# Kernel optimization log

Hardware: AMD Instinct MI355X
Metric: run time of the kernel (lower is better)

The kernel has to match this reference:

```python
import jax, jax.numpy as jnp
import numpy as np

N_NODES = 50000
N_EDGES = 800000
ATOM_DIM = 128
BOND_DIM = 16
HID = 128
STEPS = 4


def setup_inputs() -> dict:
    key = jax.random.key(0)
    k1, k2, k3, k4, k5, k6 = jax.random.split(key, 6)
    atoms = jax.random.normal(k1, (N_NODES, ATOM_DIM), dtype=jnp.float32)
    bonds = jax.random.normal(k2, (N_NODES, BOND_DIM), dtype=jnp.float32)
    pairs = jax.random.randint(k3, (N_EDGES, 2), 0, N_NODES)
    # sort rows by target id (tf.math.segment_sum expects sorted segment ids)
    order = jnp.argsort(pairs[:, 0])
    pairs = pairs[order].astype(jnp.int64)
    # learned parameters (glorot-ish scaling)
    kernel = jax.random.normal(k4, (ATOM_DIM, BOND_DIM * BOND_DIM), dtype=jnp.float32) * (2.0 / (ATOM_DIM + BOND_DIM * BOND_DIM)) ** 0.5
    bias = jnp.zeros((BOND_DIM * BOND_DIM,), dtype=jnp.float32)
    weight_node = jax.random.normal(k5, (BOND_DIM, HID), dtype=jnp.float32) * (2.0 / (BOND_DIM + HID)) ** 0.5
    weight_node_inp = jax.random.normal(k6, (BOND_DIM, HID), dtype=jnp.float32) * (2.0 / (BOND_DIM + HID)) ** 0.5
    return {"atoms": atoms, "bonds": bonds, "pairs": pairs,
            "kernel": kernel, "bias": bias,
            "weight_node": weight_node, "weight_node_inp": weight_node_inp}


def reference(atoms, bonds, pairs, kernel, bias, weight_node, weight_node_inp):
    n, bd = bonds.shape
    # per-node transform -> [N, bd, bd] message matrices
    A = (atoms @ kernel + bias).reshape(n, bd, bd)
    src = pairs[:, 0]
    nbr = pairs[:, 1]
    # gather bonds of neighbors, apply source-node matrix per edge: [E, bd]
    trans = jnp.einsum('eij,ej->ei', A[src], bonds[nbr])
    # scatter-add back to nodes keyed on pairs[:,0]
    aggregate = jax.ops.segment_sum(trans, src, num_segments=n)  # [N, bd]
    # step loop: aggregate is never updated in the original, so each step
    # computes the identical result; compute once and replicate.
    nodes = aggregate @ weight_node            # [N, hid]
    edges = jax.nn.relu(bonds @ weight_node_inp)  # [N, hid]
    result = jax.nn.relu(nodes + edges)
    return jnp.stack([result] * STEPS)  # [steps, N, hid]
```

## Files before the change

### kernel.cpp

```cpp
#include <hip/hip_runtime.h>

typedef __attribute__((ext_vector_type(8))) short bf16x8;
typedef __attribute__((ext_vector_type(4))) float f32x4;

constexpr int N       = 50000;
constexpr int NE      = 800000;
constexpr int AD      = 128;
constexpr int BD      = 16;
constexpr int BD2     = 256;
constexpr int HIDDEN  = 128;
constexpr int EPG     = 32;
constexpr int NB      = 64;

__device__ inline short f2bf(float f) {
    union U { float f; unsigned u; } v; v.f = f;
    unsigned r = v.u + 0x7fffu + ((v.u >> 16) & 1u);
    return (short)(r >> 16);
}

__global__ __launch_bounds__(256) void prep_frags(
    const float* __restrict__ kmat,
    const float* __restrict__ Wn,
    const float* __restrict__ Wi,
    short* __restrict__ kbf,
    short* __restrict__ wbf)
{
    int t = blockIdx.x * 256 + threadIdx.x;
    if (t < 4096) {
        int u = t >> 6, l = t & 63;
        int nf = u >> 2, kk = u & 3;
        int col = nf * 16 + (l & 15);
        int k0  = kk * 32 + (l >> 4) * 8;
        bf16x8 o;
#pragma unroll
        for (int j = 0; j < 8; ++j) o[j] = f2bf(kmat[(size_t)(k0 + j) * BD2 + col]);
        *(bf16x8*)(kbf + (size_t)t * 8) = o;
    } else if (t < 4096 + 1024) {
        int t2 = t - 4096;
        int u = t2 >> 6, l = t2 & 63;
        int m = u >> 3, nf2 = u & 7;
        const float* W = m ? Wi : Wn;
        int col = nf2 * 16 + (l & 15);
        int k0  = (l >> 4) * 8;
        bf16x8 o;
#pragma unroll
        for (int j = 0; j < 8; ++j) {
            int k = k0 + j;
            o[j] = (k < 16) ? f2bf(W[(size_t)k * HIDDEN + col]) : (short)0;
        }
        *(bf16x8*)(wbf + (size_t)t2 * 8) = o;
    }
}

__global__ __launch_bounds__(256) void edge_scatter_sorted(
    const int2* __restrict__ pairs,
    const float* __restrict__ bonds,
    float* __restrict__ S)
{
    const int gid = (int)((blockIdx.x * (unsigned)blockDim.x + threadIdx.x) >> 4);
    const int c   = threadIdx.x & 15;
    long e0 = (long)gid * EPG;
    if (e0 >= NE) return;

    int   cur = -1;
    float acc = 0.f;
    for (long e = e0; e < e0 + EPG; e += 4) {
        int2 pb[4]; float vb[4];
#pragma unroll
        for (int i = 0; i < 4; ++i) pb[i] = pairs[e + i];
#pragma unroll
        for (int i = 0; i < 4; ++i) vb[i] = bonds[(size_t)pb[i].y * BD + c];
#pragma unroll
        for (int i = 0; i < 4; ++i) {
            if (pb[i].x != cur) {
                if (cur >= 0) atomicAdd(&S[(size_t)cur * BD + c], acc);
                acc = 0.f;
                cur = pb[i].x;
            }
            acc += vb[i];
        }
    }
    atomicAdd(&S[(size_t)cur * BD + c], acc);
}

__global__ __launch_bounds__(256, 3) void fused_node_mfma(
    const float* __restrict__ atoms,
    const float* __restrict__ bonds,
    const short* __restrict__ kbf,
    const short* __restrict__ wbf,
    const float* __restrict__ bias,
    const float* __restrict__ S,
    float* __restrict__ out)
{
    const int tid = threadIdx.x;
    const int w   = tid >> 6;
    const int l   = tid & 63;
    const int lq  = l >> 4;
    const int lj  = l & 15;
    const int wrow = blockIdx.x * NB + w * 16;

    int arow = wrow + lj; if (arow >= N) arow = N - 1;
    const float* ap = atoms + (size_t)arow * AD + lq * 8;
    bf16x8 afrag[4];
#pragma unroll
    for (int kk = 0; kk < 4; ++kk) {
        float4 a0 = *(const float4*)(ap + kk * 32);
        float4 a1 = *(const float4*)(ap + kk * 32 + 4);
        bf16x8 af;
        af[0] = f2bf(a0.x); af[1] = f2bf(a0.y); af[2] = f2bf(a0.z); af[3] = f2bf(a0.w);
        af[4] = f2bf(a1.x); af[5] = f2bf(a1.y); af[6] = f2bf(a1.z); af[7] = f2bf(a1.w);
        afrag[kk] = af;
    }

    f32x4 acc[16];
#pragma unroll
    for (int nf = 0; nf < 16; ++nf) acc[nf] = (f32x4){0.f, 0.f, 0.f, 0.f};

    const bf16x8* kb = (const bf16x8*)kbf;
#pragma unroll 1
    for (int kk = 0; kk < 4; ++kk) {
#pragma unroll
        for (int nf = 0; nf < 16; ++nf) {
            bf16x8 b = kb[(size_t)(nf * 4 + kk) * 64 + l];
            acc[nf] = __builtin_amdgcn_mfma_f32_16x16x32_bf16(b, afrag[kk], acc[nf], 0, 0, 0);
        }
    }

    int srow = wrow + lj; if (srow >= N) srow = N - 1;
    float4 sv = *(const float4*)(S + (size_t)srow * BD + lq * 4);

    float aggf[16];
#pragma unroll
    for (int nf = 0; nf < 16; ++nf) {
        float4 bv = *(const float4*)(bias + nf * 16 + lq * 4);
        float q = (acc[nf][0] + bv.x) * sv.x
                + (acc[nf][1] + bv.y) * sv.y
                + (acc[nf][2] + bv.z) * sv.z
                + (acc[nf][3] + bv.w) * sv.w;
        q += __shfl_xor(q, 16);
        q += __shfl_xor(q, 32);
        aggf[nf] = q;
    }

    bf16x8 agg_a = (bf16x8){0,0,0,0,0,0,0,0};
    bf16x8 bond_a = (bf16x8){0,0,0,0,0,0,0,0};
    if (lq < 2) {
#pragma unroll
        for (int j = 0; j < 8; ++j) agg_a[j] = f2bf(aggf[lq * 8 + j]);
        int brow = wrow + lj; if (brow >= N) brow = N - 1;
        float4 b0 = *(const float4*)(bonds + (size_t)brow * BD + lq * 8);
        float4 b1 = *(const float4*)(bonds + (size_t)brow * BD + lq * 8 + 4);
        bond_a[0] = f2bf(b0.x); bond_a[1] = f2bf(b0.y); bond_a[2] = f2bf(b0.z); bond_a[3] = f2bf(b0.w);
        bond_a[4] = f2bf(b1.x); bond_a[5] = f2bf(b1.y); bond_a[6] = f2bf(b1.z); bond_a[7] = f2bf(b1.w);
    }

    const bf16x8* wb = (const bf16x8*)wbf;
#pragma unroll
    for (int nf2 = 0; nf2 < 8; ++nf2) {
        bf16x8 wn_f = wb[(size_t)nf2 * 64 + l];
        bf16x8 wi_f = wb[(size_t)(8 + nf2) * 64 + l];
        f32x4 e = __builtin_amdgcn_mfma_f32_16x16x32_bf16(
            bond_a, wi_f, (f32x4){0.f, 0.f, 0.f, 0.f}, 0, 0, 0);
        e[0] = fmaxf(e[0], 0.f); e[1] = fmaxf(e[1], 0.f);
        e[2] = fmaxf(e[2], 0.f); e[3] = fmaxf(e[3], 0.f);
        f32x4 o = __builtin_amdgcn_mfma_f32_16x16x32_bf16(agg_a, wn_f, e, 0, 0, 0);
#pragma unroll
        for (int r = 0; r < 4; ++r) {
            int node = wrow + 4 * lq + r;
            if (node < N) {
                float v = fmaxf(o[r], 0.f);
                size_t base = (size_t)node * HIDDEN + nf2 * 16 + lj;
#pragma unroll
                for (int s = 0; s < 4; ++s)
                    out[base + (size_t)s * N * HIDDEN] = v;
            }
        }
    }
}

extern "C" void kernel_launch(void* const* d_in, const int* in_sizes, int n_in,
                              void* d_out, int out_size, void* d_ws, size_t ws_size,
                              hipStream_t stream)
{
    const float* atoms = (const float*)d_in[0];
    const float* bonds = (const float*)d_in[1];
    const int2*  pairs = (const int2*)d_in[2];
    const float* kmat  = (const float*)d_in[3];
    const float* bias  = (const float*)d_in[4];
    const float* Wn    = (const float*)d_in[5];
    const float* Wi    = (const float*)d_in[6];
    float* out = (float*)d_out;

    float* S   = (float*)d_ws;
    short* kbf = (short*)((char*)d_ws + (size_t)N * BD * 4);
    short* wbf = kbf + 4096 * 8;

    hipMemsetAsync(S, 0, (size_t)N * BD * sizeof(float), stream);
    prep_frags<<<20, 256, 0, stream>>>(kmat, Wn, Wi, kbf, wbf);

    const int groups  = NE / EPG;
    const int threads = groups * 16;
    edge_scatter_sorted<<<(threads + 255) / 256, 256, 0, stream>>>(pairs, bonds, S);

    fused_node_mfma<<<(N + NB - 1) / NB, 256, 0, stream>>>(
        atoms, bonds, kbf, wbf, bias, S, out);
}
```

Measured before the change: 71.91 us.

## Fuse edge segment-sum into node kernel via binary search and LDS accumulation

```diff
diff --git a/kernel.cpp b/kernel.cpp
--- a/kernel.cpp
+++ b/kernel.cpp
@@ -9,8 +9,9 @@
 constexpr int BD      = 16;
 constexpr int BD2     = 256;
 constexpr int HIDDEN  = 128;
-constexpr int EPG     = 32;
 constexpr int NB      = 64;
+constexpr int SSTR    = 20;
+constexpr int OSTR    = 132;
 
 __device__ inline short f2bf(float f) {
     union U { float f; unsigned u; } v; v.f = f;
@@ -52,63 +53,102 @@
     }
 }
 
-__global__ __launch_bounds__(256) void edge_scatter_sorted(
-    const int2* __restrict__ pairs,
-    const float* __restrict__ bonds,
-    float* __restrict__ S)
-{
-    const int gid = (int)((blockIdx.x * (unsigned)blockDim.x + threadIdx.x) >> 4);
-    const int c   = threadIdx.x & 15;
-    long e0 = (long)gid * EPG;
-    if (e0 >= NE) return;
-
-    int   cur = -1;
-    float acc = 0.f;
-    for (long e = e0; e < e0 + EPG; e += 4) {
-        int2 pb[4]; float vb[4];
-#pragma unroll
-        for (int i = 0; i < 4; ++i) pb[i] = pairs[e + i];
-#pragma unroll
-        for (int i = 0; i < 4; ++i) vb[i] = bonds[(size_t)pb[i].y * BD + c];
-#pragma unroll
-        for (int i = 0; i < 4; ++i) {
-            if (pb[i].x != cur) {
-                if (cur >= 0) atomicAdd(&S[(size_t)cur * BD + c], acc);
-                acc = 0.f;
-                cur = pb[i].x;
-            }
-            acc += vb[i];
-        }
-    }
-    atomicAdd(&S[(size_t)cur * BD + c], acc);
-}
-
-__global__ __launch_bounds__(256, 3) void fused_node_mfma(
+__global__ __launch_bounds__(256, 4) void fused_all(
     const float* __restrict__ atoms,
     const float* __restrict__ bonds,
+    const int*  __restrict__ pairs,
     const short* __restrict__ kbf,
     const short* __restrict__ wbf,
     const float* __restrict__ bias,
-    const float* __restrict__ S,
     float* __restrict__ out)
 {
+    __shared__ float lds[NB * OSTR];
+
     const int tid = threadIdx.x;
     const int w   = tid >> 6;
     const int l   = tid & 63;
     const int lq  = l >> 4;
     const int lj  = l & 15;
-    const int wrow = blockIdx.x * NB + w * 16;
+    const int nb  = blockIdx.x * NB;
+    const int wrow = nb + w * 16;
 
     int arow = wrow + lj; if (arow >= N) arow = N - 1;
     const float* ap = atoms + (size_t)arow * AD + lq * 8;
+    float4 a0[4], a1[4];
+#pragma unroll
+    for (int kk = 0; kk < 4; ++kk) {
+        a0[kk] = *(const float4*)(ap + kk * 32);
+        a1[kk] = *(const float4*)(ap + kk * 32 + 4);
+    }
+
+    int wlo = nb * 16 - 4096; if (wlo < 0) wlo = 0;
+    int whi = (nb + NB) * 16 + 4096; if (whi > NE) whi = NE;
+    if (wlo > 0  && pairs[2 * wlo] >= nb)      wlo = 0;
+    if (whi < NE && pairs[2 * whi] <  nb + NB) whi = NE;
+    int eLo;
+    {
+        int s = wlo, e = whi;
+        while (s < e) { int m = (s + e) >> 1; if (pairs[2 * m] < nb) s = m + 1; else e = m; }
+        eLo = s;
+    }
+    int eHi;
+    {
+        int s = eLo, e = whi;
+        while (s < e) { int m = (s + e) >> 1; if (pairs[2 * m] < nb + NB) s = m + 1; else e = m; }
+        eHi = s;
+    }
+
+    for (int i = tid; i < NB * SSTR; i += 256) lds[i] = 0.f;
+    __syncthreads();
+
+    {
+        const int g = tid >> 4;
+        const int c = tid & 15;
+        const int nE = eHi - eLo;
+        const int cg = (nE + 15) >> 4;
+        int gs = eLo + g * cg;
+        int ge = gs + cg; if (ge > eHi) ge = eHi;
+        int cur = -1; float acc = 0.f;
+        int e = gs;
+        for (; e + 4 <= ge; e += 4) {
+            int2 pb[4]; float vb[4];
+#pragma unroll
+            for (int i = 0; i < 4; ++i) pb[i] = *(const int2*)(pairs + 2 * (e + i));
+#pragma unroll
+            for (int i = 0; i < 4; ++i) vb[i] = bonds[(size_t)pb[i].y * BD + c];
+#pragma unroll
+            for (int i = 0; i < 4; ++i) {
+                if (pb[i].x != cur) {
+                    if (cur >= 0) atomicAdd(&lds[(cur - nb) * SSTR + c], acc);
+                    acc = 0.f; cur = pb[i].x;
+                }
+                acc += vb[i];
+            }
+        }
+        for (; e < ge; ++e) {
+            int2 p = *(const int2*)(pairs + 2 * e);
+            float v = bonds[(size_t)p.y * BD + c];
+            if (p.x != cur) {
+                if (cur >= 0) atomicAdd(&lds[(cur - nb) * SSTR + c], acc);
+                acc = 0.f; cur = p.x;
+            }
+            acc += v;
+        }
+        if (cur >= 0) atomicAdd(&lds[(cur - nb) * SSTR + c], acc);
+    }
+    __syncthreads();
+
+    float4 sv = *(const float4*)(&lds[(w * 16 + lj) * SSTR + lq * 4]);
+    __syncthreads();
+
     bf16x8 afrag[4];
 #pragma unroll
     for (int kk = 0; kk < 4; ++kk) {
-        float4 a0 = *(const float4*)(ap + kk * 32);
-        float4 a1 = *(const float4*)(ap + kk * 32 + 4);
         bf16x8 af;
-        af[0] = f2bf(a0.x); af[1] = f2bf(a0.y); af[2] = f2bf(a0.z); af[3] = f2bf(a0.w);
-        af[4] = f2bf(a1.x); af[5] = f2bf(a1.y); af[6] = f2bf(a1.z); af[7] = f2bf(a1.w);
+        af[0] = f2bf(a0[kk].x); af[1] = f2bf(a0[kk].y);
+        af[2] = f2bf(a0[kk].z); af[3] = f2bf(a0[kk].w);
+        af[4] = f2bf(a1[kk].x); af[5] = f2bf(a1[kk].y);
+        af[6] = f2bf(a1[kk].z); af[7] = f2bf(a1[kk].w);
         afrag[kk] = af;
     }
 
@@ -125,9 +165,6 @@
             acc[nf] = __builtin_amdgcn_mfma_f32_16x16x32_bf16(b, afrag[kk], acc[nf], 0, 0, 0);
         }
     }
-
-    int srow = wrow + lj; if (srow >= N) srow = N - 1;
-    float4 sv = *(const float4*)(S + (size_t)srow * BD + lq * 4);
 
     float aggf[16];
 #pragma unroll
@@ -142,7 +179,7 @@
         aggf[nf] = q;
     }
 
-    bf16x8 agg_a = (bf16x8){0,0,0,0,0,0,0,0};
+    bf16x8 agg_a  = (bf16x8){0,0,0,0,0,0,0,0};
     bf16x8 bond_a = (bf16x8){0,0,0,0,0,0,0,0};
     if (lq < 2) {
 #pragma unroll
@@ -150,8 +187,10 @@
         int brow = wrow + lj; if (brow >= N) brow = N - 1;
         float4 b0 = *(const float4*)(bonds + (size_t)brow * BD + lq * 8);
         float4 b1 = *(const float4*)(bonds + (size_t)brow * BD + lq * 8 + 4);
-        bond_a[0] = f2bf(b0.x); bond_a[1] = f2bf(b0.y); bond_a[2] = f2bf(b0.z); bond_a[3] = f2bf(b0.w);
-        bond_a[4] = f2bf(b1.x); bond_a[5] = f2bf(b1.y); bond_a[6] = f2bf(b1.z); bond_a[7] = f2bf(b1.w);
+        bond_a[0] = f2bf(b0.x); bond_a[1] = f2bf(b0.y);
+        bond_a[2] = f2bf(b0.z); bond_a[3] = f2bf(b0.w);
+        bond_a[4] = f2bf(b1.x); bond_a[5] = f2bf(b1.y);
+        bond_a[6] = f2bf(b1.z); bond_a[7] = f2bf(b1.w);
     }
 
     const bf16x8* wb = (const bf16x8*)wbf;
@@ -166,13 +205,24 @@
         f32x4 o = __builtin_amdgcn_mfma_f32_16x16x32_bf16(agg_a, wn_f, e, 0, 0, 0);
 #pragma unroll
         for (int r = 0; r < 4; ++r) {
-            int node = wrow + 4 * lq + r;
-            if (node < N) {
-                float v = fmaxf(o[r], 0.f);
-                size_t base = (size_t)node * HIDDEN + nf2 * 16 + lj;
-#pragma unroll
-                for (int s = 0; s < 4; ++s)
-                    out[base + (size_t)s * N * HIDDEN] = v;
+            int nl = w * 16 + 4 * lq + r;
+            lds[nl * OSTR + nf2 * 16 + lj] = fmaxf(o[r], 0.f);
+        }
+    }
+    __syncthreads();
+
+#pragma unroll
+    for (int p = 0; p < 8; ++p) {
+        int idx  = tid + 256 * p;
+        int nl   = idx >> 5;
+        int h4   = (idx & 31) * 4;
+        int node = nb + nl;
+        if (node < N) {
+            f32x4 v = *(const f32x4*)(&lds[nl * OSTR + h4]);
+            float* dst = out + (size_t)node * HIDDEN + h4;
+#pragma unroll
+            for (int s = 0; s < 4; ++s) {
+                __builtin_nontemporal_store(v, (f32x4*)(dst + (size_t)s * N * HIDDEN));
             }
         }
     }
@@ -184,24 +234,18 @@
 {
     const float* atoms = (const float*)d_in[0];
     const float* bonds = (const float*)d_in[1];
-    const int2*  pairs = (const int2*)d_in[2];
+    const int*   pairs = (const int*)d_in[2];
     const float* kmat  = (const float*)d_in[3];
     const float* bias  = (const float*)d_in[4];
     const float* Wn    = (const float*)d_in[5];
     const float* Wi    = (const float*)d_in[6];
     float* out = (float*)d_out;
 
-    float* S   = (float*)d_ws;
-    short* kbf = (short*)((char*)d_ws + (size_t)N * BD * 4);
+    short* kbf = (short*)d_ws;
     short* wbf = kbf + 4096 * 8;
 
-    hipMemsetAsync(S, 0, (size_t)N * BD * sizeof(float), stream);
     prep_frags<<<20, 256, 0, stream>>>(kmat, Wn, Wi, kbf, wbf);
 
-    const int groups  = NE / EPG;
-    const int threads = groups * 16;
-    edge_scatter_sorted<<<(threads + 255) / 256, 256, 0, stream>>>(pairs, bonds, S);
-
-    fused_node_mfma<<<(N + NB - 1) / NB, 256, 0, stream>>>(
-        atoms, bonds, kbf, wbf, bias, S, out);
-}
+    fused_all<<<(N + NB - 1) / NB, 256, 0, stream>>>(
+        atoms, bonds, pairs, kbf, wbf, bias, out);
+}
```

New measurement: 76.60 us. +6.5%, slower.
